# Optimization experiments

Measured on AMD Instinct MI355X. Metric: run time of the kernel, lower is better.

Reference implementation:

```python
import jax, jax.numpy as jnp
import numpy as np

TOP_K = 2
TEMPERATURE = 2.0


def setup_inputs() -> dict:
    key = jax.random.key(0)
    k1, k2, k3 = jax.random.split(key, 3)
    x = jax.random.normal(k1, (16384, 2048), dtype=jnp.float32)
    gate_w = jax.random.normal(k2, (64, 2048), dtype=jnp.float32) * 0.02
    gate_b = jax.random.normal(k3, (64,), dtype=jnp.float32) * 0.02
    expert_maturity = jnp.ones((64,), dtype=jnp.int32)  # all mature -> top-k branch
    return {"x": x, "gate_w": gate_w, "gate_b": gate_b, "expert_maturity": expert_maturity}


def _routing(logits, expert_maturity):
    # branch 1: any immature expert -> temperature softmax over all experts
    def soft_branch(lg):
        return jax.nn.softmax(lg / TEMPERATURE, axis=-1)

    # branch 2: all mature -> top-k selection, softmax over selected, scatter into zeros
    def topk_branch(lg):
        top_w, top_idx = jax.lax.top_k(lg, TOP_K)          # [N, K]
        top_sm = jax.nn.softmax(top_w, axis=-1)            # [N, K]
        n = lg.shape[0]
        rows = jnp.arange(n)[:, None]                      # [N, 1]
        return jnp.zeros_like(lg).at[rows, top_idx].set(top_sm)

    any_immature = jnp.any(expert_maturity == 0)
    return jax.lax.cond(any_immature, soft_branch, topk_branch, logits)


def reference(x, gate_w, gate_b, expert_maturity):
    # logits = x @ W^T + b : [N, E]
    logits = jnp.einsum("nd,ed->ne", x, gate_w) + gate_b
    return _routing(logits, expert_maturity)
```

## Files before the change

kernel.cpp:

```cpp
#include <hip/hip_runtime.h>
#include <math.h>


#define NROWS 16384
#define DIM   2048
#define NEXP  64
#define BM    32
#define TPB   512
#define KSLICE 256
#define KSTEPS (KSLICE / 32)

typedef __attribute__((ext_vector_type(4))) float f32x4;
typedef __attribute__((ext_vector_type(8))) short bf16x8;

__global__ void wfrag_kernel(const float* __restrict__ gw,
                             unsigned short* __restrict__ wsH,
                             unsigned short* __restrict__ wsL) {
  int slot  = blockIdx.x * 256 + threadIdx.x;
  int lane  = slot & 63;
  int t     = (slot >> 6) & 3;
  int kstep = slot >> 8;
  int e  = 16 * t + (lane & 15);
  int k0 = kstep * 32 + (lane >> 4) * 8;
  const float* src = gw + (size_t)e * DIM + k0;
  bf16x8 vh, vl;
#pragma unroll
  for (int j = 0; j < 8; ++j) {
    float w = src[j];
    unsigned u = __float_as_uint(w);
    vh[j] = (short)(u >> 16);
    float hi = __uint_as_float(u & 0xffff0000u);
    float rl = w - hi;
    vl[j] = (short)(__float_as_uint(rl) >> 16);
  }
  ((bf16x8*)wsH)[slot] = vh;
  ((bf16x8*)wsL)[slot] = vl;
}

__global__ __launch_bounds__(TPB, 4)
void router_mfma(const float* __restrict__ x,
                 const unsigned short* __restrict__ wsH,
                 const unsigned short* __restrict__ wsL,
                 const float* __restrict__ gb,
                 const int* __restrict__ mat,
                 float* __restrict__ out) {
  __shared__ float slab[4 * BM * NEXP];
  __shared__ float p_a[BM], p_b[BM];
  __shared__ int   p_i[BM], p_j[BM];
  __shared__ int   s_flag;

  const int tid  = threadIdx.x;
  const int wave = tid >> 6;
  const int lane = tid & 63;
  const int m    = lane & 15;
  const int kg   = lane >> 4;
  const int row0 = blockIdx.x * BM;

  if (tid < 64) {
    unsigned long long b = __ballot(mat[lane] == 0);
    if (lane == 0) s_flag = (b != 0ull) ? 1 : 0;
  }

  f32x4 acc[2][4];
#pragma unroll
  for (int r = 0; r < 2; ++r)
#pragma unroll
    for (int t = 0; t < 4; ++t) acc[r][t] = (f32x4)0.0f;

  const bf16x8* bHp = (const bf16x8*)wsH + (size_t)(wave * KSTEPS * 4) * 64 + lane;
  const bf16x8* bLp = (const bf16x8*)wsL + (size_t)(wave * KSTEPS * 4) * 64 + lane;

  const float* xb = x + (size_t)(row0 + m) * DIM + wave * KSLICE + kg * 8;

  float4 xr[2][2];
  xr[0][0] = *(const float4*)(xb);
  xr[0][1] = *(const float4*)(xb + 4);
  xr[1][0] = *(const float4*)(xb + 16 * DIM);
  xr[1][1] = *(const float4*)(xb + 16 * DIM + 4);

#pragma unroll
  for (int s = 0; s < KSTEPS; ++s) {
    bf16x8 ah[2], al[2];
#pragma unroll
    for (int r = 0; r < 2; ++r) {
#pragma unroll
      for (int q = 0; q < 2; ++q) {
        float4 v = xr[r][q];
        float f0 = v.x, f1 = v.y, f2 = v.z, f3 = v.w;
        float ff[4] = {f0, f1, f2, f3};
#pragma unroll
        for (int j = 0; j < 4; ++j) {
          unsigned u = __float_as_uint(ff[j]);
          ah[r][q * 4 + j] = (short)(u >> 16);
          float hi = __uint_as_float(u & 0xffff0000u);
          float rl = ff[j] - hi;
          al[r][q * 4 + j] = (short)(__float_as_uint(rl) >> 16);
        }
      }
    }
    bf16x8 bh[4], bl[4];
#pragma unroll
    for (int t = 0; t < 4; ++t) {
      bh[t] = bHp[(size_t)s * 256 + t * 64];
      bl[t] = bLp[(size_t)s * 256 + t * 64];
    }
    if (s + 1 < KSTEPS) {
      const float* xn = xb + (s + 1) * 32;
      xr[0][0] = *(const float4*)(xn);
      xr[0][1] = *(const float4*)(xn + 4);
      xr[1][0] = *(const float4*)(xn + 16 * DIM);
      xr[1][1] = *(const float4*)(xn + 16 * DIM + 4);
    }
#pragma unroll
    for (int r = 0; r < 2; ++r) {
#pragma unroll
      for (int t = 0; t < 4; ++t) {
        acc[r][t] = __builtin_amdgcn_mfma_f32_16x16x32_bf16(ah[r], bh[t], acc[r][t], 0, 0, 0);
        acc[r][t] = __builtin_amdgcn_mfma_f32_16x16x32_bf16(ah[r], bl[t], acc[r][t], 0, 0, 0);
        acc[r][t] = __builtin_amdgcn_mfma_f32_16x16x32_bf16(al[r], bh[t], acc[r][t], 0, 0, 0);
      }
    }
  }

  if (wave >= 4) {
    float* sl = slab + (wave - 4) * (BM * NEXP);
#pragma unroll
    for (int r = 0; r < 2; ++r)
#pragma unroll
      for (int t = 0; t < 4; ++t)
#pragma unroll
        for (int reg = 0; reg < 4; ++reg)
          sl[(16 * r + kg * 4 + reg) * NEXP + 16 * t + m] = acc[r][t][reg];
  }
  __syncthreads();
  if (wave < 4) {
    float* sl = slab + wave * (BM * NEXP);
#pragma unroll
    for (int r = 0; r < 2; ++r)
#pragma unroll
      for (int t = 0; t < 4; ++t)
#pragma unroll
        for (int reg = 0; reg < 4; ++reg)
          sl[(16 * r + kg * 4 + reg) * NEXP + 16 * t + m] += acc[r][t][reg];
  }
  __syncthreads();
  for (int idx = tid; idx < BM * NEXP; idx += TPB) {
    float v = slab[idx] + slab[2048 + idx] + slab[4096 + idx] + slab[6144 + idx]
            + gb[idx & (NEXP - 1)];
    slab[idx] = v;
  }
  __syncthreads();

  const int flag = s_flag;

  if (tid < BM) {
    const float* rowp = slab + tid * NEXP;
    if (flag == 0) {
      float m1 = -1e30f, m2 = -1e30f;
      int i1 = 0, i2 = 0;
      for (int ee = 0; ee < NEXP; ++ee) {
        int e = (ee + tid) & (NEXP - 1);
        float v = rowp[e];
        if (v > m1) { m2 = m1; i2 = i1; m1 = v; i1 = e; }
        else if (v > m2) { m2 = v; i2 = e; }
      }
      float t = expf(m2 - m1);
      float pa = 1.0f / (1.0f + t);
      p_a[tid] = pa;
      p_b[tid] = t * pa;
      p_i[tid] = i1;
      p_j[tid] = i2;
    } else {
      float mx = -1e30f;
      for (int ee = 0; ee < NEXP; ++ee)
        mx = fmaxf(mx, rowp[(ee + tid) & (NEXP - 1)]);
      float ssum = 0.0f;
      for (int ee = 0; ee < NEXP; ++ee)
        ssum += expf((rowp[(ee + tid) & (NEXP - 1)] - mx) * 0.5f);
      p_a[tid] = mx;
      p_b[tid] = 1.0f / ssum;
    }
  }
  __syncthreads();

  {
    int q  = tid;
    int r  = q >> 4;
    int e0 = (q & 15) * 4;
    float4 v;
    if (flag == 0) {
      int i1 = p_i[r], i2 = p_j[r];
      float a = p_a[r], b = p_b[r];
      v.x = (e0 + 0 == i1) ? a : (e0 + 0 == i2) ? b : 0.0f;
      v.y = (e0 + 1 == i1) ? a : (e0 + 1 == i2) ? b : 0.0f;
      v.z = (e0 + 2 == i1) ? a : (e0 + 2 == i2) ? b : 0.0f;
      v.w = (e0 + 3 == i1) ? a : (e0 + 3 == i2) ? b : 0.0f;
    } else {
      float mx = p_a[r], inv = p_b[r];
      const float* rowp = slab + r * NEXP + e0;
      v.x = expf((rowp[0] - mx) * 0.5f) * inv;
      v.y = expf((rowp[1] - mx) * 0.5f) * inv;
      v.z = expf((rowp[2] - mx) * 0.5f) * inv;
      v.w = expf((rowp[3] - mx) * 0.5f) * inv;
    }
    *(float4*)(out + (size_t)(row0 + r) * NEXP + e0) = v;
  }
}

extern "C" void kernel_launch(void* const* d_in, const int* in_sizes, int n_in,
                              void* d_out, int out_size, void* d_ws, size_t ws_size,
                              hipStream_t stream) {
  const float* x  = (const float*)d_in[0];
  const float* gw = (const float*)d_in[1];
  const float* gb = (const float*)d_in[2];
  const int*   mt = (const int*)d_in[3];
  float* outp = (float*)d_out;
  (void)in_sizes; (void)n_in; (void)out_size; (void)ws_size;

  unsigned short* wsH = (unsigned short*)d_ws;
  unsigned short* wsL = wsH + 64 * DIM;

  wfrag_kernel<<<64, 256, 0, stream>>>(gw, wsH, wsL);
  router_mfma<<<NROWS / BM, TPB, 0, stream>>>(x, wsH, wsL, gb, mt, outp);
}
```

Measured before the change: 210.4 us.

## Split waves across expert halves with longer K slices and prefetch weight fragments

Changes the per-block work split so each pair of waves shares a 512-wide K slice and each wave covers half the experts, instead of 8 waves each covering a 256-wide K slice and all 64 experts. Each x element is now converted to bf16 hi/lo by two waves, which duplicates conversion work and global reads of x. In exchange, accumulator registers are halved and the second slab accumulation pass with its extra barrier is removed. Weight fragments are software-prefetched one step ahead, and the launch-bounds occupancy hint is lowered from 4 to 3.

```diff
diff --git a/kernel.cpp b/kernel.cpp
--- a/kernel.cpp
+++ b/kernel.cpp
@@ -7,7 +7,7 @@
 #define NEXP  64
 #define BM    32
 #define TPB   512
-#define KSLICE 256
+#define KSLICE 512
 #define KSTEPS (KSLICE / 32)
 
 typedef __attribute__((ext_vector_type(4))) float f32x4;
@@ -37,7 +37,7 @@
   ((bf16x8*)wsL)[slot] = vl;
 }
 
-__global__ __launch_bounds__(TPB, 4)
+__global__ __launch_bounds__(TPB, 3)
 void router_mfma(const float* __restrict__ x,
                  const unsigned short* __restrict__ wsH,
                  const unsigned short* __restrict__ wsL,
@@ -51,6 +51,8 @@
 
   const int tid  = threadIdx.x;
   const int wave = tid >> 6;
+  const int ksl  = wave >> 1;
+  const int eh   = wave & 1;
   const int lane = tid & 63;
   const int m    = lane & 15;
   const int kg   = lane >> 4;
@@ -61,22 +63,29 @@
     if (lane == 0) s_flag = (b != 0ull) ? 1 : 0;
   }
 
-  f32x4 acc[2][4];
+  f32x4 acc[2][2];
 #pragma unroll
   for (int r = 0; r < 2; ++r)
 #pragma unroll
-    for (int t = 0; t < 4; ++t) acc[r][t] = (f32x4)0.0f;
-
-  const bf16x8* bHp = (const bf16x8*)wsH + (size_t)(wave * KSTEPS * 4) * 64 + lane;
-  const bf16x8* bLp = (const bf16x8*)wsL + (size_t)(wave * KSTEPS * 4) * 64 + lane;
-
-  const float* xb = x + (size_t)(row0 + m) * DIM + wave * KSLICE + kg * 8;
+    for (int t = 0; t < 2; ++t) acc[r][t] = (f32x4)0.0f;
+
+  const size_t bbase = (size_t)(((ksl * KSTEPS) * 4 + 2 * eh) * 64 + lane);
+  const bf16x8* bHp = (const bf16x8*)wsH + bbase;
+  const bf16x8* bLp = (const bf16x8*)wsL + bbase;
+
+  const float* xb = x + (size_t)(row0 + m) * DIM + ksl * KSLICE + kg * 8;
 
   float4 xr[2][2];
   xr[0][0] = *(const float4*)(xb);
   xr[0][1] = *(const float4*)(xb + 4);
   xr[1][0] = *(const float4*)(xb + 16 * DIM);
   xr[1][1] = *(const float4*)(xb + 16 * DIM + 4);
+  bf16x8 bhc[2], blc[2];
+#pragma unroll
+  for (int t = 0; t < 2; ++t) {
+    bhc[t] = bHp[t * 64];
+    blc[t] = bLp[t * 64];
+  }
 
 #pragma unroll
   for (int s = 0; s < KSTEPS; ++s) {
@@ -86,8 +95,7 @@
 #pragma unroll
       for (int q = 0; q < 2; ++q) {
         float4 v = xr[r][q];
-        float f0 = v.x, f1 = v.y, f2 = v.z, f3 = v.w;
-        float ff[4] = {f0, f1, f2, f3};
+        float ff[4] = {v.x, v.y, v.z, v.w};
 #pragma unroll
         for (int j = 0; j < 4; ++j) {
           unsigned u = __float_as_uint(ff[j]);
@@ -98,52 +106,45 @@
         }
       }
     }
-    bf16x8 bh[4], bl[4];
-#pragma unroll
-    for (int t = 0; t < 4; ++t) {
-      bh[t] = bHp[(size_t)s * 256 + t * 64];
-      bl[t] = bLp[(size_t)s * 256 + t * 64];
-    }
-    if (s + 1 < KSTEPS) {
-      const float* xn = xb + (s + 1) * 32;
+    const int sn = (s + 1 < KSTEPS) ? (s + 1) : s;
+    {
+      const float* xn = xb + sn * 32;
       xr[0][0] = *(const float4*)(xn);
       xr[0][1] = *(const float4*)(xn + 4);
       xr[1][0] = *(const float4*)(xn + 16 * DIM);
       xr[1][1] = *(const float4*)(xn + 16 * DIM + 4);
     }
+    bf16x8 bhn[2], bln[2];
+#pragma unroll
+    for (int t = 0; t < 2; ++t) {
+      bhn[t] = bHp[(size_t)sn * 256 + t * 64];
+      bln[t] = bLp[(size_t)sn * 256 + t * 64];
+    }
 #pragma unroll
     for (int r = 0; r < 2; ++r) {
 #pragma unroll
-      for (int t = 0; t < 4; ++t) {
-        acc[r][t] = __builtin_amdgcn_mfma_f32_16x16x32_bf16(ah[r], bh[t], acc[r][t], 0, 0, 0);
-        acc[r][t] = __builtin_amdgcn_mfma_f32_16x16x32_bf16(ah[r], bl[t], acc[r][t], 0, 0, 0);
-        acc[r][t] = __builtin_amdgcn_mfma_f32_16x16x32_bf16(al[r], bh[t], acc[r][t], 0, 0, 0);
+      for (int t = 0; t < 2; ++t) {
+        acc[r][t] = __builtin_amdgcn_mfma_f32_16x16x32_bf16(ah[r], bhc[t], acc[r][t], 0, 0, 0);
+        acc[r][t] = __builtin_amdgcn_mfma_f32_16x16x32_bf16(ah[r], blc[t], acc[r][t], 0, 0, 0);
+        acc[r][t] = __builtin_amdgcn_mfma_f32_16x16x32_bf16(al[r], bhc[t], acc[r][t], 0, 0, 0);
       }
     }
-  }
-
-  if (wave >= 4) {
-    float* sl = slab + (wave - 4) * (BM * NEXP);
+#pragma unroll
+    for (int t = 0; t < 2; ++t) { bhc[t] = bhn[t]; blc[t] = bln[t]; }
+  }
+
+  {
+    float* sl = slab + ksl * (BM * NEXP);
 #pragma unroll
     for (int r = 0; r < 2; ++r)
 #pragma unroll
-      for (int t = 0; t < 4; ++t)
+      for (int t = 0; t < 2; ++t)
 #pragma unroll
         for (int reg = 0; reg < 4; ++reg)
-          sl[(16 * r + kg * 4 + reg) * NEXP + 16 * t + m] = acc[r][t][reg];
+          sl[(16 * r + kg * 4 + reg) * NEXP + 32 * eh + 16 * t + m] = acc[r][t][reg];
   }
   __syncthreads();
-  if (wave < 4) {
-    float* sl = slab + wave * (BM * NEXP);
-#pragma unroll
-    for (int r = 0; r < 2; ++r)
-#pragma unroll
-      for (int t = 0; t < 4; ++t)
-#pragma unroll
-        for (int reg = 0; reg < 4; ++reg)
-          sl[(16 * r + kg * 4 + reg) * NEXP + 16 * t + m] += acc[r][t][reg];
-  }
-  __syncthreads();
+
   for (int idx = tid; idx < BM * NEXP; idx += TPB) {
     float v = slab[idx] + slab[2048 + idx] + slab[4096 + idx] + slab[6144 + idx]
             + gb[idx & (NEXP - 1)];
```

After: 218.7 us. 1.04x slower.
